# Kernel tuning notes

Hardware: AMD Instinct MI355X
Metric: run time of the kernel (lower is better)

Reference implementation:

```python
import jax, jax.numpy as jnp
import numpy as np

N, E = 50000, 800000
NODE_IN, EDGE_IN = 32, 16
EMB, GEMB = 128, 128
H, C, L, B = 4, 32, 2, 8   # heads, per-head dim, layers, graphs
GAT_IN = NODE_IN + EMB      # skip_conn=True
NEG_SLOPE = 0.2
EPS = 1e-5


def layernorm(x, g, b):
    m = jnp.mean(x, -1, keepdims=True)
    v = jnp.mean((x - m) ** 2, -1, keepdims=True)
    return (x - m) / jnp.sqrt(v + EPS) * g + b


def setup_inputs() -> dict:
    key = jax.random.key(0)
    ks = jax.random.split(key, 24)
    s = 0.05
    return {
        "x": jax.random.normal(ks[0], (N, NODE_IN), jnp.float32),
        "edge_attr": jax.random.normal(ks[1], (E, EDGE_IN), jnp.float32),
        "W_in": jax.random.normal(ks[2], (NODE_IN, EMB), jnp.float32) * s,
        "b_in": jnp.zeros((EMB,), jnp.float32),
        "W_src": jax.random.normal(ks[3], (L, GAT_IN, H * C), jnp.float32) * s,
        "W_edge": jax.random.normal(ks[4], (L, EDGE_IN, H * C), jnp.float32) * s,
        "att_src": jax.random.normal(ks[5], (L, H, C), jnp.float32) * s,
        "att_dst": jax.random.normal(ks[6], (L, H, C), jnp.float32) * s,
        "att_edge": jax.random.normal(ks[7], (L, H, C), jnp.float32) * s,
        "gat_bias": jnp.zeros((L, H * C), jnp.float32),
        "ln_gamma": jnp.ones((L, EMB), jnp.float32),
        "ln_beta": jnp.zeros((L, EMB), jnp.float32),
        "W_out": jax.random.normal(ks[8], (EMB, EMB), jnp.float32) * s,
        "b_out": jnp.zeros((EMB,), jnp.float32),
        "ln_out_gamma": jnp.ones((EMB,), jnp.float32),
        "ln_out_beta": jnp.zeros((EMB,), jnp.float32),
        "W_g": jax.random.normal(ks[9], (EMB, GEMB), jnp.float32) * s,
        "b_g": jnp.zeros((GEMB,), jnp.float32),
        "g_gamma": jnp.ones((GEMB,), jnp.float32),
        "g_beta": jnp.zeros((GEMB,), jnp.float32),
        "edge_index": jax.random.randint(ks[10], (2, E), 0, N, jnp.int32),
        "batch": jnp.sort(jax.random.randint(ks[11], (N,), 0, B, jnp.int32)),
    }


def reference(x, edge_attr, W_in, b_in, W_src, W_edge, att_src, att_dst, att_edge,
              gat_bias, ln_gamma, ln_beta, W_out, b_out, ln_out_gamma, ln_out_beta,
              W_g, b_g, g_gamma, g_beta, edge_index, batch):
    # PyG GATConv adds self-loops with edge_attr fill_value='mean'
    loop = jnp.arange(N, dtype=edge_index.dtype)
    src = jnp.concatenate([edge_index[0], loop])   # [E2]
    dst = jnp.concatenate([edge_index[1], loop])   # [E2]
    ea = jnp.concatenate([edge_attr, jnp.broadcast_to(edge_attr.mean(0), (N, EDGE_IN))], 0)

    h = jax.nn.relu(x @ W_in + b_in)  # [N, EMB]
    for l in range(L):
        inp = jnp.concatenate([x, h], -1)                   # skip connection [N, GAT_IN]
        xs = (inp @ W_src[l]).reshape(N, H, C)              # projected nodes
        a_s = jnp.einsum('nhc,hc->nh', xs, att_src[l])
        a_d = jnp.einsum('nhc,hc->nh', xs, att_dst[l])
        ee = (ea @ W_edge[l]).reshape(-1, H, C)             # [E2, H, C]
        a_e = jnp.einsum('ehc,hc->eh', ee, att_edge[l])
        alpha = jax.nn.leaky_relu(a_s[src] + a_d[dst] + a_e, NEG_SLOPE)  # [E2, H]
        # segment softmax over incoming edges of each destination node
        amax = jax.ops.segment_max(alpha, dst, num_segments=N)
        ex = jnp.exp(alpha - amax[dst])
        denom = jax.ops.segment_sum(ex, dst, num_segments=N)
        w = ex / (denom[dst] + 1e-16)
        msg = xs[src] * w[:, :, None]                        # [E2, H, C]
        out = jax.ops.segment_sum(msg, dst, num_segments=N).reshape(N, H * C) + gat_bias[l]
        h = jax.nn.elu(layernorm(out, ln_gamma[l], ln_beta[l]))

    g = layernorm(jax.nn.relu(h @ W_g + b_g), g_gamma, g_beta)
    gsum = jax.ops.segment_sum(g, batch, num_segments=B)
    cnt = jax.ops.segment_sum(jnp.ones((N, 1), g.dtype), batch, num_segments=B)
    graph_embeddings = gsum / jnp.maximum(cnt, 1.0)

    node_embeddings = layernorm(jax.nn.relu(h @ W_out + b_out), ln_out_gamma, ln_out_beta)
    return node_embeddings, graph_embeddings
```

## Files before the change

### kernel.cpp

```cpp
#include <hip/hip_runtime.h>

#define N_NODES 50000
#define N_EDGES 800000
#define E2      850000
#define NODE_IN 32
#define EDGE_IN 16
#define EMB     128
#define GAT_IN  160
#define NLAYER  2
#define NGRAPH  8
#define NB32    1563
#define NB64    782
#define EB      3321
#define LOG2E   1.44269504088896340736f

#define NBUCK   98
#define CHUNK   4096
#define NCHUNK  208

#define GWT_SRC0 0
#define GWT_SRC1 20480
#define GWT_OUT  40960
#define GWT_G    57344
#define GWT_TOT  73728

typedef short bf16x8 __attribute__((ext_vector_type(8)));
typedef float f32x4 __attribute__((ext_vector_type(4)));

__device__ __forceinline__ unsigned int f2bf(float f) {
    unsigned int u = __float_as_uint(f);
    return (u + 0x7FFFu + ((u >> 16) & 1u)) >> 16;
}
__device__ __forceinline__ float bf2f(unsigned int h) {
    return __uint_as_float(h << 16);
}
__device__ __forceinline__ unsigned int pack2bf(float a, float b) {
    return f2bf(a) | (f2bf(b) << 16);
}

__global__ void zero_kernel(float* __restrict__ p, int n) {
    int i = blockIdx.x * blockDim.x + threadIdx.x;
    int stride = gridDim.x * blockDim.x;
    for (; i < n; i += stride) p[i] = 0.f;
}

__global__ __launch_bounds__(256) void mega_kernel(
    const int* __restrict__ edge_index, const float* __restrict__ edge_attr,
    const float* __restrict__ x, const float* __restrict__ W_in,
    const float* __restrict__ b_in,
    const float* __restrict__ Wsrc, const float* __restrict__ Wout,
    const float* __restrict__ Wg,
    int* __restrict__ hist, float* __restrict__ meta,
    unsigned int* __restrict__ h_bf, unsigned int* __restrict__ x_bf,
    unsigned short* __restrict__ gwt) {
    __shared__ float smem[32 * NODE_IN];
    int b = blockIdx.x, t = threadIdx.x;

    if (b < NCHUNK) {
        int* lh = (int*)smem;
        if (t < NBUCK) lh[t] = 0;
        __syncthreads();
        int c0 = b * CHUNK;
#pragma unroll
        for (int i = 0; i < CHUNK / 256; i++) {
            int e = c0 + i * 256 + t;
            if (e < E2) {
                int dst = (e < N_EDGES) ? edge_index[N_EDGES + e] : (e - N_EDGES);
                atomicAdd(&lh[dst >> 9], 1);
            }
        }
        __syncthreads();
        if (t < NBUCK) hist[t * NCHUNK + b] = lh[t];
    } else if (b < NCHUNK + 512) {
        if (t < 16) smem[t] = 0.f;
        __syncthreads();
        int gid = (b - NCHUNK) * 256 + t;
        int q = gid & 3;
        const float4* ea4 = (const float4*)edge_attr;
        float4 s = make_float4(0.f, 0.f, 0.f, 0.f);
        for (int j = gid; j < N_EDGES * 4; j += 512 * 256) {
            float4 v = ea4[j];
            s.x += v.x; s.y += v.y; s.z += v.z; s.w += v.w;
        }
        atomicAdd(&smem[q * 4 + 0], s.x);
        atomicAdd(&smem[q * 4 + 1], s.y);
        atomicAdd(&smem[q * 4 + 2], s.z);
        atomicAdd(&smem[q * 4 + 3], s.w);
        __syncthreads();
        if (t < 16) atomicAdd(&meta[t], smem[t]);
    } else if (b < NCHUNK + 512 + NB32) {
        float (*inp)[NODE_IN] = (float (*)[NODE_IN])smem;
        int n0 = (b - NCHUNK - 512) * 32;
        for (int i = t; i < 32 * NODE_IN; i += 256) {
            int r = i >> 5, c = i & 31;
            int n = min(n0 + r, N_NODES - 1);
            inp[r][c] = x[(size_t)n * NODE_IN + c];
        }
        __syncthreads();
        for (int i = t; i < 32 * 16; i += 256) {
            int r = i >> 4, c = i & 15;
            int n = n0 + r;
            if (n < N_NODES) x_bf[(size_t)n * 16 + c] = pack2bf(inp[r][2 * c], inp[r][2 * c + 1]);
        }
        int wave = t >> 6, lane = t & 63;
        int c0 = lane * 2, c1 = c0 + 1;
        const float2* W2 = (const float2*)W_in;
        float acc[8][2];
#pragma unroll
        for (int j = 0; j < 8; j++) { acc[j][0] = b_in[c0]; acc[j][1] = b_in[c1]; }
#pragma unroll 2
        for (int k4 = 0; k4 < NODE_IN / 4; k4++) {
            float4 v[8];
#pragma unroll
            for (int j = 0; j < 8; j++) v[j] = *(const float4*)&inp[wave * 8 + j][k4 * 4];
#pragma unroll
            for (int kk = 0; kk < 4; kk++) {
                float2 w = W2[(k4 * 4 + kk) * 64 + lane];
#pragma unroll
                for (int j = 0; j < 8; j++) {
                    float vv = (&v[j].x)[kk];
                    acc[j][0] += vv * w.x;
                    acc[j][1] += vv * w.y;
                }
            }
        }
#pragma unroll
        for (int j = 0; j < 8; j++) {
            int n = n0 + wave * 8 + j;
            if (n < N_NODES)
                h_bf[(size_t)n * 64 + lane] = pack2bf(fmaxf(acc[j][0], 0.f), fmaxf(acc[j][1], 0.f));
        }
    } else {
        int g = (b - NCHUNK - 512 - NB32) * 256 + t;
        const float* Wm;
        int base, gg;
        if (g < 5120) {
            int l = g / 2560;
            gg = g - l * 2560;
            Wm = Wsrc + (size_t)l * GAT_IN * EMB;
            base = l * 20480;
        } else if (g < 7168) {
            gg = g - 5120;
            Wm = Wout;
            base = GWT_OUT;
        } else {
            gg = g - 7168;
            Wm = Wg;
            base = GWT_G;
        }
        int lane = gg & 63, tmp = gg >> 6;
        int nt = tmp & 7, kc = tmp >> 3;
        int quad = lane >> 4, l16 = lane & 15;
        int col = nt * 16 + l16, k0 = kc * 32 + quad * 8;
        unsigned int u[4];
#pragma unroll
        for (int j = 0; j < 4; j++)
            u[j] = pack2bf(Wm[(size_t)(k0 + 2 * j) * EMB + col],
                           Wm[(size_t)(k0 + 2 * j + 1) * EMB + col]);
        *(uint4*)(gwt + base + (size_t)gg * 8) = make_uint4(u[0], u[1], u[2], u[3]);
    }
}

__global__ __launch_bounds__(256) void bucket_scan_kernel(int* __restrict__ hist,
                                                          int* __restrict__ btot) {
    __shared__ int sm[256];
    int k = blockIdx.x, t = threadIdx.x;
    int v = (t < NCHUNK) ? hist[k * NCHUNK + t] : 0;
    sm[t] = v;
    __syncthreads();
#pragma unroll
    for (int d = 1; d < 256; d <<= 1) {
        int u = (t >= d) ? sm[t - d] : 0;
        __syncthreads();
        sm[t] += u;
        __syncthreads();
    }
    if (t < NCHUNK) hist[k * NCHUNK + t] = sm[t] - v;
    if (t == 255) btot[k] = sm[255];
}

__global__ __launch_bounds__(256) void base_prep_kernel(const int* __restrict__ btot,
                                                        int* __restrict__ bucket_base,
                                                        const float* __restrict__ W_edge,
                                                        const float* __restrict__ att_edge,
                                                        float* __restrict__ meta) {
    __shared__ int sm[256];
    int t = threadIdx.x;
    int v = (t < NBUCK) ? btot[t] : 0;
    sm[t] = v;
    __syncthreads();
#pragma unroll
    for (int d = 1; d < 256; d <<= 1) {
        int u = (t >= d) ? sm[t - d] : 0;
        __syncthreads();
        sm[t] += u;
        __syncthreads();
    }
    if (t < NBUCK) bucket_base[t] = sm[t] - v;
    if (t == NBUCK - 1) bucket_base[NBUCK] = sm[t];

    if (t < EDGE_IN) meta[t] = meta[t] * (1.0f / (float)N_EDGES);
    __syncthreads();
    if (t < 128) {
        int l = t >> 6, k = (t >> 2) & 15, h = t & 3;
        const float* w = W_edge + ((size_t)l * EDGE_IN + k) * EMB + h * 32;
        const float* a = att_edge + (size_t)l * EMB + h * 32;
        float acc = 0.f;
#pragma unroll
        for (int c = 0; c < 32; c++) acc += w[c] * a[c];
        meta[16 + (l * 16 + k) * 4 + h] = acc * LOG2E;
    }
    __syncthreads();
    if (t < 8) {
        int l = t >> 2, h = t & 3;
        float acc = 0.f;
#pragma unroll
        for (int k = 0; k < EDGE_IN; k++) acc += meta[k] * meta[16 + (l * 16 + k) * 4 + h];
        meta[144 + t] = acc;
    }
}

__global__ __launch_bounds__(256) void scatter_bucket_kernel(const int* __restrict__ edge_index,
                                                             const int* __restrict__ hist,
                                                             const int* __restrict__ bucket_base,
                                                             int2* __restrict__ brec) {
    __shared__ int cur[NBUCK];
    int b = blockIdx.x, t = threadIdx.x;
    if (t < NBUCK) cur[t] = bucket_base[t] + hist[t * NCHUNK + b];
    __syncthreads();
    int c0 = b * CHUNK;
#pragma unroll
    for (int i = 0; i < CHUNK / 256; i++) {
        int e = c0 + i * 256 + t;
        if (e < E2) {
            int src, dst;
            if (e < N_EDGES) {
                src = edge_index[e];
                dst = edge_index[N_EDGES + e];
            } else {
                src = dst = e - N_EDGES;
            }
            int pos = atomicAdd(&cur[dst >> 9], 1);
            brec[pos] = make_int2(src | ((dst & 511) << 16), e);
        }
    }
}

__global__ __launch_bounds__(512) void local_sort_kernel(const int* __restrict__ bucket_base,
                                                         const int2* __restrict__ brec,
                                                         int* __restrict__ off,
                                                         int2* __restrict__ perm) {
    __shared__ int lh[512];
    __shared__ int sm[512];
    int k = blockIdx.x, t = threadIdx.x;
    int base = bucket_base[k], end = bucket_base[k + 1], cnt = end - base;
    lh[t] = 0;
    __syncthreads();
    for (int i = t; i < cnt; i += 512) {
        int2 r = brec[base + i];
        atomicAdd(&lh[(r.x >> 16) & 511], 1);
    }
    __syncthreads();
    int v = lh[t];
    sm[t] = v;
    __syncthreads();
#pragma unroll
    for (int d = 1; d < 512; d <<= 1) {
        int u = (t >= d) ? sm[t - d] : 0;
        __syncthreads();
        sm[t] += u;
        __syncthreads();
    }
    int excl = sm[t] - v;
    int dst = (k << 9) + t;
    if (dst < N_NODES) off[dst] = base + excl;
    if (k == NBUCK - 1 && t == 0) off[N_NODES] = E2;
    lh[t] = excl;
    __syncthreads();
    for (int i = t; i < cnt; i += 512) {
        int2 r = brec[base + i];
        int dl = (r.x >> 16) & 511;
        int p = atomicAdd(&lh[dl], 1);
        perm[base + p] = make_int2(r.x & 0xFFFF, r.y);
    }
}

__global__ __launch_bounds__(256) void compute_ae_kernel(const int2* __restrict__ perm,
                                                         const float* __restrict__ edge_attr,
                                                         const float* __restrict__ meta,
                                                         int* __restrict__ csr_src,
                                                         float* __restrict__ csr_ae0,
                                                         float* __restrict__ csr_ae1) {
    __shared__ float Ml[128];
    __shared__ float loop_ae[8];
    int t = threadIdx.x;
    if (t < 128) Ml[t] = meta[16 + t];
    if (t < 8) loop_ae[t] = meta[144 + t];
    __syncthreads();
    int p = blockIdx.x * 256 + t;
    if (p >= E2) return;
    int2 pe = perm[p];
    int src = pe.x, e = pe.y;
    csr_src[p] = src;
    float ae[2][4];
    if (e < N_EDGES) {
        const float4* r4 = (const float4*)(edge_attr + (size_t)e * EDGE_IN);
#pragma unroll
        for (int l = 0; l < 2; l++)
#pragma unroll
            for (int hh = 0; hh < 4; hh++) ae[l][hh] = 0.f;
#pragma unroll
        for (int q = 0; q < 4; q++) {
            float4 v = r4[q];
#pragma unroll
            for (int l = 0; l < 2; l++) {
                const float* M = Ml + l * 64;
#pragma unroll
                for (int hh = 0; hh < 4; hh++) {
                    ae[l][hh] += v.x * M[(4 * q + 0) * 4 + hh] + v.y * M[(4 * q + 1) * 4 + hh] +
                                 v.z * M[(4 * q + 2) * 4 + hh] + v.w * M[(4 * q + 3) * 4 + hh];
                }
            }
        }
    } else {
#pragma unroll
        for (int l = 0; l < 2; l++)
#pragma unroll
            for (int hh = 0; hh < 4; hh++) ae[l][hh] = loop_ae[l * 4 + hh];
    }
    *(float4*)(csr_ae0 + (size_t)p * 4) = make_float4(ae[0][0], ae[0][1], ae[0][2], ae[0][3]);
    *(float4*)(csr_ae1 + (size_t)p * 4) = make_float4(ae[1][0], ae[1][1], ae[1][2], ae[1][3]);
}

template <int K, int MODE>
__global__ __launch_bounds__(256) void dense_mfma_kernel(
    const unsigned int* __restrict__ xbf, const unsigned int* __restrict__ hbf,
    const unsigned short* __restrict__ gwt, const float* __restrict__ bias,
    const float* __restrict__ v1, const float* __restrict__ v2,
    const int* __restrict__ batch,
    unsigned int* __restrict__ xs_out, float* __restrict__ a_s, float* __restrict__ a_d,
    float* __restrict__ out_nodes, float* __restrict__ gsum, float* __restrict__ gcnt) {
    constexpr int CLS = 132;
    __shared__ __align__(16) float cl[64 * CLS];
    __shared__ float red[(MODE != 0) ? 64 : 1][8];
    __shared__ float locw[(MODE == 2) ? 4 : 1][2][EMB];
    __shared__ int bids[(MODE == 2) ? 64 : 1];

    int t = threadIdx.x;
    int n0 = blockIdx.x * 64;
    if (MODE == 2 && t < 64) bids[t] = batch[min(n0 + t, N_NODES - 1)];

    int wave = t >> 6, lane = t & 63;
    int quad = lane >> 4, l16 = lane & 15;
    int arow = min(n0 + wave * 16 + l16, N_NODES - 1);
    const bf16x8* B = (const bf16x8*)gwt;
    f32x4 acc[8];
#pragma unroll
    for (int i = 0; i < 8; i++) acc[i] = (f32x4){0.f, 0.f, 0.f, 0.f};
#pragma unroll
    for (int kc = 0; kc < K / 32; kc++) {
        bf16x8 af;
        if (MODE == 0 && kc == 0) {
            af = *(const bf16x8*)(xbf + (size_t)arow * 16 + quad * 4);
        } else {
            int hk = ((MODE == 0) ? (kc - 1) : kc) * 16;
            af = *(const bf16x8*)(hbf + (size_t)arow * 64 + hk + quad * 4);
        }
#pragma unroll
        for (int nt = 0; nt < 8; nt++) {
            bf16x8 bfv = B[(kc * 8 + nt) * 64 + lane];
            acc[nt] = __builtin_amdgcn_mfma_f32_16x16x32_bf16(af, bfv, acc[nt], 0, 0, 0);
        }
    }
#pragma unroll
    for (int nt = 0; nt < 8; nt++) {
#pragma unroll
        for (int i = 0; i < 4; i++) {
            int r = wave * 16 + quad * 4 + i;
            cl[r * CLS + nt * 16 + l16] = acc[nt][i];
        }
    }
    __syncthreads();

    int p = t & 3, r = t >> 2;
    int n = n0 + r;
    const float4* c4 = (const float4*)(cl + r * CLS + p * 32);

    if (MODE == 0) {
        const float4* s4 = (const float4*)(v1 + p * 32);
        const float4* d4 = (const float4*)(v2 + p * 32);
        if (n < N_NODES) {
            float s_ = 0.f, d_ = 0.f;
#pragma unroll
            for (int i = 0; i < 8; i++) {
                float4 cv = c4[i], sv = s4[i], dv = d4[i];
                s_ += cv.x * sv.x + cv.y * sv.y + cv.z * sv.z + cv.w * sv.w;
                d_ += cv.x * dv.x + cv.y * dv.y + cv.z * dv.z + cv.w * dv.w;
                uint2 pk = make_uint2(pack2bf(cv.x, cv.y), pack2bf(cv.z, cv.w));
                *(uint2*)(xs_out + (size_t)n * 64 + p * 16 + 2 * i) = pk;
            }
            a_s[(size_t)n * 4 + p] = s_ * LOG2E;
            a_d[(size_t)n * 4 + p] = d_ * LOG2E;
        }
    } else {
        const float4* b4 = (const float4*)(bias + p * 32);
        float vals[32];
        float s_ = 0.f, q_ = 0.f;
#pragma unroll
        for (int i = 0; i < 8; i++) {
            float4 cv = c4[i], bv = b4[i];
            float w0 = fmaxf(cv.x + bv.x, 0.f), w1 = fmaxf(cv.y + bv.y, 0.f);
            float w2 = fmaxf(cv.z + bv.z, 0.f), w3 = fmaxf(cv.w + bv.w, 0.f);
            vals[4 * i] = w0; vals[4 * i + 1] = w1; vals[4 * i + 2] = w2; vals[4 * i + 3] = w3;
            s_ += w0 + w1 + w2 + w3;
            q_ += w0 * w0 + w1 * w1 + w2 * w2 + w3 * w3;
        }
        red[r][p] = s_;
        red[r][4 + p] = q_;
        __syncthreads();
        float sm = red[r][0] + red[r][1] + red[r][2] + red[r][3];
        float sq = red[r][4] + red[r][5] + red[r][6] + red[r][7];
        float mean = sm * (1.f / EMB);
        float var = sq * (1.f / EMB) - mean * mean;
        float rstd = rsqrtf(var + 1e-5f);
        const float4* g4 = (const float4*)(v1 + p * 32);
        const float4* be4 = (const float4*)(v2 + p * 32);
#pragma unroll
        for (int i = 0; i < 8; i++) {
            float4 gv = g4[i], bv = be4[i];
            vals[4 * i]     = (vals[4 * i]     - mean) * rstd * gv.x + bv.x;
            vals[4 * i + 1] = (vals[4 * i + 1] - mean) * rstd * gv.y + bv.y;
            vals[4 * i + 2] = (vals[4 * i + 2] - mean) * rstd * gv.z + bv.z;
            vals[4 * i + 3] = (vals[4 * i + 3] - mean) * rstd * gv.w + bv.w;
        }
        if (MODE == 1) {
            if (n < N_NODES) {
                float* op = out_nodes + (size_t)n * EMB + p * 32;
#pragma unroll
                for (int i = 0; i < 8; i++)
                    *(float4*)(op + 4 * i) = make_float4(vals[4 * i], vals[4 * i + 1],
                                                         vals[4 * i + 2], vals[4 * i + 3]);
            }
        } else {
            int nvalid = min(64, N_NODES - n0);
            int bmin = bids[0], bmax = bids[nvalid - 1];
            int bid = bids[r];
            bool inA = (bid == bmin) && (n < N_NODES);
            bool inB = (bid == bmax) && (bmax != bmin) && (n < N_NODES);
            if (n < N_NODES && bid != bmin && bid != bmax) {
#pragma unroll
                for (int i = 0; i < 32; i++)
                    atomicAdd(&gsum[(size_t)bid * EMB + p * 32 + i], vals[i]);
            }
#pragma unroll
            for (int g = 0; g < 2; g++) {
                bool m = g ? inB : inA;
#pragma unroll
                for (int i = 0; i < 32; i++) {
                    float v = m ? vals[i] : 0.f;
                    v += __shfl_xor(v, 4, 64);
                    v += __shfl_xor(v, 8, 64);
                    v += __shfl_xor(v, 16, 64);
                    v += __shfl_xor(v, 32, 64);
                    if ((lane >> 2) == 0) locw[wave][g][(lane & 3) * 32 + i] = v;
                }
            }
            __syncthreads();
            if (t < 128) {
                float sA = locw[0][0][t] + locw[1][0][t] + locw[2][0][t] + locw[3][0][t];
                atomicAdd(&gsum[(size_t)bmin * EMB + t], sA);
                if (bmax != bmin) {
                    float sB = locw[0][1][t] + locw[1][1][t] + locw[2][1][t] + locw[3][1][t];
                    atomicAdd(&gsum[(size_t)bmax * EMB + t], sB);
                }
            } else if (t == 255) {
                int cA = 0, cB = 0;
                for (int rr = 0; rr < nvalid; rr++) {
                    int bb = bids[rr];
                    if (bb == bmin) cA++;
                    else if (bb == bmax) cB++;
                    else atomicAdd(&gcnt[bb], 1.f);
                }
                atomicAdd(&gcnt[bmin], (float)cA);
                if (bmax != bmin && cB > 0) atomicAdd(&gcnt[bmax], (float)cB);
            }
        }
    }
}

__global__ __launch_bounds__(256) void gat_gather_kernel(const int* __restrict__ off,
                                                         const int* __restrict__ csr_src,
                                                         const float* __restrict__ csr_ae,
                                                         const unsigned int* __restrict__ xs,
                                                         const float* __restrict__ a_s,
                                                         const float* __restrict__ a_d,
                                                         const float* __restrict__ bias_l,
                                                         const float* __restrict__ gamma_l,
                                                         const float* __restrict__ beta_l,
                                                         unsigned int* __restrict__ h_bf) {
    int t = threadIdx.x, wave = t >> 6, lane = t & 63;
    int n = blockIdx.x * 4 + wave;
    int g = lane >> 4, l16 = lane & 15;
    int h = l16 >> 2;
    float ad = a_d[n * 4 + h];
    int p0 = __builtin_amdgcn_readfirstlane(off[n]);
    int p1 = __builtin_amdgcn_readfirstlane(off[n + 1]);
    float den = 0.f;
    float acc[8];
#pragma unroll
    for (int j = 0; j < 8; j++) acc[j] = 0.f;

#define ACCUM8(X, EX)                                          \
    acc[0] += EX * __uint_as_float(X.x << 16);                 \
    acc[1] += EX * __uint_as_float(X.x & 0xFFFF0000u);         \
    acc[2] += EX * __uint_as_float(X.y << 16);                 \
    acc[3] += EX * __uint_as_float(X.y & 0xFFFF0000u);         \
    acc[4] += EX * __uint_as_float(X.z << 16);                 \
    acc[5] += EX * __uint_as_float(X.z & 0xFFFF0000u);         \
    acc[6] += EX * __uint_as_float(X.w << 16);                 \
    acc[7] += EX * __uint_as_float(X.w & 0xFFFF0000u);

    int pb = p0;
    for (; pb + 8 <= p1; pb += 8) {
        int pA = pb + g, pB = pA + 4;
        int sA = csr_src[pA], sB = csr_src[pB];
        float aeA = csr_ae[pA * 4 + h];
        float aeB = csr_ae[pB * 4 + h];
        float asA = a_s[sA * 4 + h];
        float asB = a_s[sB * 4 + h];
        uint4 xA = *(const uint4*)(xs + (sA * 64 + l16 * 4));
        uint4 xB = *(const uint4*)(xs + (sB * 64 + l16 * 4));
        float alA = asA + ad + aeA;
        alA = fmaxf(alA, 0.2f * alA);
        float exA = exp2f(alA);
        float alB = asB + ad + aeB;
        alB = fmaxf(alB, 0.2f * alB);
        float exB = exp2f(alB);
        den += exA + exB;
        ACCUM8(xA, exA)
        ACCUM8(xB, exB)
    }
    if (pb < p1) {
        int plast = p1 - 1;
        int qA = pb + g, qB = pb + 4 + g;
        int pA = min(qA, plast), pB = min(qB, plast);
        int sA = csr_src[pA], sB = csr_src[pB];
        float aeA = csr_ae[pA * 4 + h];
        float aeB = csr_ae[pB * 4 + h];
        float asA = a_s[sA * 4 + h];
        float asB = a_s[sB * 4 + h];
        uint4 xA = *(const uint4*)(xs + (sA * 64 + l16 * 4));
        uint4 xB = *(const uint4*)(xs + (sB * 64 + l16 * 4));
        float alA = asA + ad + aeA;
        alA = fmaxf(alA, 0.2f * alA);
        float exA = (qA <= plast) ? exp2f(alA) : 0.f;
        float alB = asB + ad + aeB;
        alB = fmaxf(alB, 0.2f * alB);
        float exB = (qB <= plast) ? exp2f(alB) : 0.f;
        den += exA + exB;
        ACCUM8(xA, exA)
        ACCUM8(xB, exB)
    }
#undef ACCUM8

#pragma unroll
    for (int j = 0; j < 8; j++) {
        acc[j] += __shfl_xor(acc[j], 16, 64);
        acc[j] += __shfl_xor(acc[j], 32, 64);
    }
    den += __shfl_xor(den, 16, 64);
    den += __shfl_xor(den, 32, 64);

    float dinv = 1.0f / (den + 1e-16f);
    int c0 = l16 * 8;
    const float4* b4 = (const float4*)(bias_l + c0);
    float4 bv0 = b4[0], bv1 = b4[1];
    float v[8];
    v[0] = acc[0] * dinv + bv0.x; v[1] = acc[1] * dinv + bv0.y;
    v[2] = acc[2] * dinv + bv0.z; v[3] = acc[3] * dinv + bv0.w;
    v[4] = acc[4] * dinv + bv1.x; v[5] = acc[5] * dinv + bv1.y;
    v[6] = acc[6] * dinv + bv1.z; v[7] = acc[7] * dinv + bv1.w;
    float sm = 0.f, sq = 0.f;
#pragma unroll
    for (int j = 0; j < 8; j++) { sm += v[j]; sq += v[j] * v[j]; }
#pragma unroll
    for (int o = 1; o <= 8; o <<= 1) {
        sm += __shfl_xor(sm, o, 64);
        sq += __shfl_xor(sq, o, 64);
    }
    float mean = sm * (1.f / EMB);
    float var = sq * (1.f / EMB) - mean * mean;
    float rstd = rsqrtf(var + 1e-5f);
    const float4* g4 = (const float4*)(gamma_l + c0);
    const float4* be4 = (const float4*)(beta_l + c0);
    float4 gv0 = g4[0], gv1 = g4[1], bev0 = be4[0], bev1 = be4[1];
    float y[8];
    y[0] = (v[0] - mean) * rstd * gv0.x + bev0.x;
    y[1] = (v[1] - mean) * rstd * gv0.y + bev0.y;
    y[2] = (v[2] - mean) * rstd * gv0.z + bev0.z;
    y[3] = (v[3] - mean) * rstd * gv0.w + bev0.w;
    y[4] = (v[4] - mean) * rstd * gv1.x + bev1.x;
    y[5] = (v[5] - mean) * rstd * gv1.y + bev1.y;
    y[6] = (v[6] - mean) * rstd * gv1.z + bev1.z;
    y[7] = (v[7] - mean) * rstd * gv1.w + bev1.w;
#pragma unroll
    for (int j = 0; j < 8; j++) y[j] = y[j] > 0.f ? y[j] : __expf(y[j]) - 1.f;
    if (g == 0) {
        uint4 o4;
        o4.x = pack2bf(y[0], y[1]);
        o4.y = pack2bf(y[2], y[3]);
        o4.z = pack2bf(y[4], y[5]);
        o4.w = pack2bf(y[6], y[7]);
        *(uint4*)(h_bf + (size_t)n * 64 + l16 * 4) = o4;
    }
}

__global__ void graph_out_kernel(const float* __restrict__ gsum, const float* __restrict__ gcnt,
                                 float* __restrict__ out) {
    int i = blockIdx.x * blockDim.x + threadIdx.x;
    if (i >= NGRAPH * EMB) return;
    int b = i >> 7;
    float c = fmaxf(gcnt[b], 1.f);
    out[(size_t)N_NODES * EMB + i] = gsum[i] / c;
}

extern "C" void kernel_launch(void* const* d_in, const int* in_sizes, int n_in,
                              void* d_out, int out_size, void* d_ws, size_t ws_size,
                              hipStream_t stream) {
    (void)in_sizes; (void)n_in; (void)out_size; (void)ws_size;
    const float* x         = (const float*)d_in[0];
    const float* edge_attr = (const float*)d_in[1];
    const float* W_in      = (const float*)d_in[2];
    const float* b_in      = (const float*)d_in[3];
    const float* W_src     = (const float*)d_in[4];
    const float* W_edge    = (const float*)d_in[5];
    const float* att_src   = (const float*)d_in[6];
    const float* att_dst   = (const float*)d_in[7];
    const float* att_edge  = (const float*)d_in[8];
    const float* gat_bias  = (const float*)d_in[9];
    const float* ln_gamma  = (const float*)d_in[10];
    const float* ln_beta   = (const float*)d_in[11];
    const float* W_out     = (const float*)d_in[12];
    const float* b_out     = (const float*)d_in[13];
    const float* ln_og     = (const float*)d_in[14];
    const float* ln_ob     = (const float*)d_in[15];
    const float* W_g       = (const float*)d_in[16];
    const float* b_g       = (const float*)d_in[17];
    const float* g_gamma   = (const float*)d_in[18];
    const float* g_beta    = (const float*)d_in[19];
    const int* edge_index  = (const int*)d_in[20];
    const int* batch       = (const int*)d_in[21];
    float* out = (float*)d_out;

    float* ws              = (float*)d_ws;
    unsigned int* h_bf     = (unsigned int*)ws;
    unsigned int* xs       = h_bf + (size_t)N_NODES * 64;
    unsigned int* x_bf     = xs + (size_t)N_NODES * 64;
    float* a_s             = (float*)(x_bf + (size_t)N_NODES * 16);
    float* a_d             = a_s + (size_t)N_NODES * 4;
    float* csr_ae          = a_d + (size_t)N_NODES * 4;
    unsigned short* gwt    = (unsigned short*)(csr_ae + (size_t)2 * E2 * 4);
    float* meta            = (float*)(gwt + GWT_TOT);
    float* gsum            = meta + 152;
    float* gcnt            = gsum + NGRAPH * EMB;
    int*   off             = (int*)(gcnt + NGRAPH);
    int*   csr_src         = off + N_NODES + 2;
    int2*  brec            = (int2*)(csr_src + E2);
    int*   hist            = (int*)(brec + E2);
    int*   btot            = hist + NBUCK * NCHUNK;
    int*   bucket_base     = btot + NBUCK;
    int2*  perm            = (int2*)xs;

    zero_kernel<<<8, 256, 0, stream>>>(meta, 152 + NGRAPH * EMB + NGRAPH);
    mega_kernel<<<NCHUNK + 512 + NB32 + 36, 256, 0, stream>>>(
        edge_index, edge_attr, x, W_in, b_in, W_src, W_out, W_g,
        hist, meta, h_bf, x_bf, gwt);

    bucket_scan_kernel<<<NBUCK, 256, 0, stream>>>(hist, btot);
    base_prep_kernel<<<1, 256, 0, stream>>>(btot, bucket_base, W_edge, att_edge, meta);
    scatter_bucket_kernel<<<NCHUNK, 256, 0, stream>>>(edge_index, hist, bucket_base, brec);
    local_sort_kernel<<<NBUCK, 512, 0, stream>>>(bucket_base, brec, off, perm);
    compute_ae_kernel<<<EB, 256, 0, stream>>>(perm, edge_attr, meta,
                                              csr_src, csr_ae, csr_ae + (size_t)E2 * 4);

    for (int l = 0; l < NLAYER; l++) {
        dense_mfma_kernel<GAT_IN, 0><<<NB64, 256, 0, stream>>>(
            x_bf, h_bf, gwt + (l ? GWT_SRC1 : GWT_SRC0), nullptr,
            att_src + (size_t)l * EMB, att_dst + (size_t)l * EMB, nullptr,
            xs, a_s, a_d, nullptr, nullptr, nullptr);
        gat_gather_kernel<<<N_NODES / 4, 256, 0, stream>>>(
            off, csr_src, csr_ae + (size_t)l * E2 * 4, xs, a_s, a_d,
            gat_bias + (size_t)l * EMB, ln_gamma + (size_t)l * EMB,
            ln_beta + (size_t)l * EMB, h_bf);
    }

    dense_mfma_kernel<EMB, 1><<<NB64, 256, 0, stream>>>(
        nullptr, h_bf, gwt + GWT_OUT, b_out, ln_og, ln_ob, nullptr,
        nullptr, nullptr, nullptr, out, nullptr, nullptr);
    dense_mfma_kernel<EMB, 2><<<NB64, 256, 0, stream>>>(
        nullptr, h_bf, gwt + GWT_G, b_g, g_gamma, g_beta, batch,
        nullptr, nullptr, nullptr, nullptr, gsum, gcnt);
    graph_out_kernel<<<4, 256, 0, stream>>>(gsum, gcnt, out);
}
```

Before: 403.7 us.

## Fuse edge-attr projection into local sort, merge output dense kernels, prefetch gather indices

Folds the per-edge attention-term computation into the local sort kernel so the intermediate perm array is never written or reread, removing one launch. The two final dense MFMA kernels (node output and graph pooling) are combined into one launch that picks its mode per block. The gather loop now software-prefetches the next iteration's source indices and edge terms to hide latency. The fused sort kernel runs with only 98 blocks, so the edge-attr work gets much less parallelism than the old 3321-block kernel did.

```diff
diff --git a/kernel.cpp b/kernel.cpp
--- a/kernel.cpp
+++ b/kernel.cpp
@@ -11,7 +11,6 @@
 #define NGRAPH  8
 #define NB32    1563
 #define NB64    782
-#define EB      3321
 #define LOG2E   1.44269504088896340736f
 
 #define NBUCK   98
@@ -248,11 +247,19 @@
 
 __global__ __launch_bounds__(512) void local_sort_kernel(const int* __restrict__ bucket_base,
                                                          const int2* __restrict__ brec,
+                                                         const float* __restrict__ edge_attr,
+                                                         const float* __restrict__ meta,
                                                          int* __restrict__ off,
-                                                         int2* __restrict__ perm) {
+                                                         int* __restrict__ csr_src,
+                                                         float* __restrict__ csr_ae0,
+                                                         float* __restrict__ csr_ae1) {
     __shared__ int lh[512];
     __shared__ int sm[512];
+    __shared__ float Ml[128];
+    __shared__ float loop_ae[8];
     int k = blockIdx.x, t = threadIdx.x;
+    if (t < 128) Ml[t] = meta[16 + t];
+    if (t < 8) loop_ae[t] = meta[144 + t];
     int base = bucket_base[k], end = bucket_base[k + 1], cnt = end - base;
     lh[t] = 0;
     __syncthreads();
@@ -281,55 +288,39 @@
         int2 r = brec[base + i];
         int dl = (r.x >> 16) & 511;
         int p = atomicAdd(&lh[dl], 1);
-        perm[base + p] = make_int2(r.x & 0xFFFF, r.y);
-    }
-}
-
-__global__ __launch_bounds__(256) void compute_ae_kernel(const int2* __restrict__ perm,
-                                                         const float* __restrict__ edge_attr,
-                                                         const float* __restrict__ meta,
-                                                         int* __restrict__ csr_src,
-                                                         float* __restrict__ csr_ae0,
-                                                         float* __restrict__ csr_ae1) {
-    __shared__ float Ml[128];
-    __shared__ float loop_ae[8];
-    int t = threadIdx.x;
-    if (t < 128) Ml[t] = meta[16 + t];
-    if (t < 8) loop_ae[t] = meta[144 + t];
-    __syncthreads();
-    int p = blockIdx.x * 256 + t;
-    if (p >= E2) return;
-    int2 pe = perm[p];
-    int src = pe.x, e = pe.y;
-    csr_src[p] = src;
-    float ae[2][4];
-    if (e < N_EDGES) {
-        const float4* r4 = (const float4*)(edge_attr + (size_t)e * EDGE_IN);
-#pragma unroll
-        for (int l = 0; l < 2; l++)
-#pragma unroll
-            for (int hh = 0; hh < 4; hh++) ae[l][hh] = 0.f;
-#pragma unroll
-        for (int q = 0; q < 4; q++) {
-            float4 v = r4[q];
-#pragma unroll
-            for (int l = 0; l < 2; l++) {
-                const float* M = Ml + l * 64;
-#pragma unroll
-                for (int hh = 0; hh < 4; hh++) {
-                    ae[l][hh] += v.x * M[(4 * q + 0) * 4 + hh] + v.y * M[(4 * q + 1) * 4 + hh] +
-                                 v.z * M[(4 * q + 2) * 4 + hh] + v.w * M[(4 * q + 3) * 4 + hh];
+        int pos = base + p;
+        int src = r.x & 0xFFFF;
+        int e = r.y;
+        csr_src[pos] = src;
+        float ae[2][4];
+        if (e < N_EDGES) {
+            const float4* r4 = (const float4*)(edge_attr + (size_t)e * EDGE_IN);
+#pragma unroll
+            for (int l = 0; l < 2; l++)
+#pragma unroll
+                for (int hh = 0; hh < 4; hh++) ae[l][hh] = 0.f;
+#pragma unroll
+            for (int q = 0; q < 4; q++) {
+                float4 vv = r4[q];
+#pragma unroll
+                for (int l = 0; l < 2; l++) {
+                    const float* M = Ml + l * 64;
+#pragma unroll
+                    for (int hh = 0; hh < 4; hh++) {
+                        ae[l][hh] += vv.x * M[(4 * q + 0) * 4 + hh] + vv.y * M[(4 * q + 1) * 4 + hh] +
+                                     vv.z * M[(4 * q + 2) * 4 + hh] + vv.w * M[(4 * q + 3) * 4 + hh];
+                    }
                 }
             }
-        }
-    } else {
-#pragma unroll
-        for (int l = 0; l < 2; l++)
-#pragma unroll
-            for (int hh = 0; hh < 4; hh++) ae[l][hh] = loop_ae[l * 4 + hh];
-    }
-    *(float4*)(csr_ae0 + (size_t)p * 4) = make_float4(ae[0][0], ae[0][1], ae[0][2], ae[0][3]);
-    *(float4*)(csr_ae1 + (size_t)p * 4) = make_float4(ae[1][0], ae[1][1], ae[1][2], ae[1][3]);
+        } else {
+#pragma unroll
+            for (int l = 0; l < 2; l++)
+#pragma unroll
+                for (int hh = 0; hh < 4; hh++) ae[l][hh] = loop_ae[l * 4 + hh];
+        }
+        *(float4*)(csr_ae0 + (size_t)pos * 4) = make_float4(ae[0][0], ae[0][1], ae[0][2], ae[0][3]);
+        *(float4*)(csr_ae1 + (size_t)pos * 4) = make_float4(ae[1][0], ae[1][1], ae[1][2], ae[1][3]);
+    }
 }
 
 template <int K, int MODE>
@@ -339,21 +330,37 @@
     const float* __restrict__ v1, const float* __restrict__ v2,
     const int* __restrict__ batch,
     unsigned int* __restrict__ xs_out, float* __restrict__ a_s, float* __restrict__ a_d,
-    float* __restrict__ out_nodes, float* __restrict__ gsum, float* __restrict__ gcnt) {
+    float* __restrict__ out_nodes, float* __restrict__ gsum, float* __restrict__ gcnt,
+    const float* __restrict__ bias2, const float* __restrict__ v1b,
+    const float* __restrict__ v2b) {
     constexpr int CLS = 132;
     __shared__ __align__(16) float cl[64 * CLS];
     __shared__ float red[(MODE != 0) ? 64 : 1][8];
-    __shared__ float locw[(MODE == 2) ? 4 : 1][2][EMB];
-    __shared__ int bids[(MODE == 2) ? 64 : 1];
+    __shared__ float locw[(MODE == 3) ? 4 : 1][2][EMB];
+    __shared__ int bids[(MODE == 3) ? 64 : 1];
 
     int t = threadIdx.x;
-    int n0 = blockIdx.x * 64;
-    if (MODE == 2 && t < 64) bids[t] = batch[min(n0 + t, N_NODES - 1)];
+    int mode = MODE;
+    int blk = blockIdx.x;
+    if (MODE == 3) {
+        mode = (blockIdx.x < NB64) ? 1 : 2;
+        blk = (mode == 1) ? blockIdx.x : blockIdx.x - NB64;
+    }
+    int n0 = blk * 64;
+    const unsigned short* gw = gwt;
+    const float* bias_ = bias;
+    const float* v1_ = v1;
+    const float* v2_ = v2;
+    if (MODE == 3 && mode == 2) {
+        gw = gwt + (GWT_G - GWT_OUT);
+        bias_ = bias2; v1_ = v1b; v2_ = v2b;
+    }
+    if (MODE == 3 && mode == 2 && t < 64) bids[t] = batch[min(n0 + t, N_NODES - 1)];
 
     int wave = t >> 6, lane = t & 63;
     int quad = lane >> 4, l16 = lane & 15;
     int arow = min(n0 + wave * 16 + l16, N_NODES - 1);
-    const bf16x8* B = (const bf16x8*)gwt;
+    const bf16x8* B = (const bf16x8*)gw;
     f32x4 acc[8];
 #pragma unroll
     for (int i = 0; i < 8; i++) acc[i] = (f32x4){0.f, 0.f, 0.f, 0.f};
@@ -387,8 +394,8 @@
     const float4* c4 = (const float4*)(cl + r * CLS + p * 32);
 
     if (MODE == 0) {
-        const float4* s4 = (const float4*)(v1 + p * 32);
-        const float4* d4 = (const float4*)(v2 + p * 32);
+        const float4* s4 = (const float4*)(v1_ + p * 32);
+        const float4* d4 = (const float4*)(v2_ + p * 32);
         if (n < N_NODES) {
             float s_ = 0.f, d_ = 0.f;
 #pragma unroll
@@ -403,7 +410,7 @@
             a_d[(size_t)n * 4 + p] = d_ * LOG2E;
         }
     } else {
-        const float4* b4 = (const float4*)(bias + p * 32);
+        const float4* b4 = (const float4*)(bias_ + p * 32);
         float vals[32];
         float s_ = 0.f, q_ = 0.f;
 #pragma unroll
@@ -423,8 +430,8 @@
         float mean = sm * (1.f / EMB);
         float var = sq * (1.f / EMB) - mean * mean;
         float rstd = rsqrtf(var + 1e-5f);
-        const float4* g4 = (const float4*)(v1 + p * 32);
-        const float4* be4 = (const float4*)(v2 + p * 32);
+        const float4* g4 = (const float4*)(v1_ + p * 32);
+        const float4* be4 = (const float4*)(v2_ + p * 32);
 #pragma unroll
         for (int i = 0; i < 8; i++) {
             float4 gv = g4[i], bv = be4[i];
@@ -433,7 +440,7 @@
             vals[4 * i + 2] = (vals[4 * i + 2] - mean) * rstd * gv.z + bv.z;
             vals[4 * i + 3] = (vals[4 * i + 3] - mean) * rstd * gv.w + bv.w;
         }
-        if (MODE == 1) {
+        if (mode == 1) {
             if (n < N_NODES) {
                 float* op = out_nodes + (size_t)n * EMB + p * 32;
 #pragma unroll
@@ -520,20 +527,36 @@
     acc[6] += EX * __uint_as_float(X.w << 16);                 \
     acc[7] += EX * __uint_as_float(X.w & 0xFFFF0000u);
 
+    int niter = (p1 - p0) >> 3;
     int pb = p0;
-    for (; pb + 8 <= p1; pb += 8) {
+    int sA = 0, sB = 0;
+    float aeA = 0.f, aeB = 0.f;
+    if (niter > 0) {
         int pA = pb + g, pB = pA + 4;
-        int sA = csr_src[pA], sB = csr_src[pB];
-        float aeA = csr_ae[pA * 4 + h];
-        float aeB = csr_ae[pB * 4 + h];
-        float asA = a_s[sA * 4 + h];
-        float asB = a_s[sB * 4 + h];
-        uint4 xA = *(const uint4*)(xs + (sA * 64 + l16 * 4));
-        uint4 xB = *(const uint4*)(xs + (sB * 64 + l16 * 4));
-        float alA = asA + ad + aeA;
+        sA = csr_src[pA];
+        sB = csr_src[pB];
+        aeA = csr_ae[pA * 4 + h];
+        aeB = csr_ae[pB * 4 + h];
+    }
+    for (int it = 0; it < niter; it++) {
+        int sA0 = sA, sB0 = sB;
+        float aeA0 = aeA, aeB0 = aeB;
+        pb += 8;
+        if (it + 1 < niter) {
+            int pA = pb + g, pB = pA + 4;
+            sA = csr_src[pA];
+            sB = csr_src[pB];
+            aeA = csr_ae[pA * 4 + h];
+            aeB = csr_ae[pB * 4 + h];
+        }
+        float asA = a_s[sA0 * 4 + h];
+        float asB = a_s[sB0 * 4 + h];
+        uint4 xA = *(const uint4*)(xs + (sA0 * 64 + l16 * 4));
+        uint4 xB = *(const uint4*)(xs + (sB0 * 64 + l16 * 4));
+        float alA = asA + ad + aeA0;
         alA = fmaxf(alA, 0.2f * alA);
         float exA = exp2f(alA);
-        float alB = asB + ad + aeB;
+        float alB = asB + ad + aeB0;
         alB = fmaxf(alB, 0.2f * alB);
         float exB = exp2f(alB);
         den += exA + exB;
@@ -544,17 +567,17 @@
         int plast = p1 - 1;
         int qA = pb + g, qB = pb + 4 + g;
         int pA = min(qA, plast), pB = min(qB, plast);
-        int sA = csr_src[pA], sB = csr_src[pB];
-        float aeA = csr_ae[pA * 4 + h];
-        float aeB = csr_ae[pB * 4 + h];
-        float asA = a_s[sA * 4 + h];
-        float asB = a_s[sB * 4 + h];
-        uint4 xA = *(const uint4*)(xs + (sA * 64 + l16 * 4));
-        uint4 xB = *(const uint4*)(xs + (sB * 64 + l16 * 4));
-        float alA = asA + ad + aeA;
+        int tsA = csr_src[pA], tsB = csr_src[pB];
+        float aeA1 = csr_ae[pA * 4 + h];
+        float aeB1 = csr_ae[pB * 4 + h];
+        float asA = a_s[tsA * 4 + h];
+        float asB = a_s[tsB * 4 + h];
+        uint4 xA = *(const uint4*)(xs + (tsA * 64 + l16 * 4));
+        uint4 xB = *(const uint4*)(xs + (tsB * 64 + l16 * 4));
+        float alA = asA + ad + aeA1;
         alA = fmaxf(alA, 0.2f * alA);
         float exA = (qA <= plast) ? exp2f(alA) : 0.f;
-        float alB = asB + ad + aeB;
+        float alB = asB + ad + aeB1;
         alB = fmaxf(alB, 0.2f * alB);
         float exB = (qB <= plast) ? exp2f(alB) : 0.f;
         den += exA + exB;
@@ -669,7 +692,6 @@
     int*   hist            = (int*)(brec + E2);
     int*   btot            = hist + NBUCK * NCHUNK;
     int*   bucket_base     = btot + NBUCK;
-    int2*  perm            = (int2*)xs;
 
     zero_kernel<<<8, 256, 0, stream>>>(meta, 152 + NGRAPH * EMB + NGRAPH);
     mega_kernel<<<NCHUNK + 512 + NB32 + 36, 256, 0, stream>>>(
@@ -679,26 +701,23 @@
     bucket_scan_kernel<<<NBUCK, 256, 0, stream>>>(hist, btot);
     base_prep_kernel<<<1, 256, 0, stream>>>(btot, bucket_base, W_edge, att_edge, meta);
     scatter_bucket_kernel<<<NCHUNK, 256, 0, stream>>>(edge_index, hist, bucket_base, brec);
-    local_sort_kernel<<<NBUCK, 512, 0, stream>>>(bucket_base, brec, off, perm);
-    compute_ae_kernel<<<EB, 256, 0, stream>>>(perm, edge_attr, meta,
-                                              csr_src, csr_ae, csr_ae + (size_t)E2 * 4);
+    local_sort_kernel<<<NBUCK, 512, 0, stream>>>(bucket_base, brec, edge_attr, meta,
+                                                 off, csr_src, csr_ae,
+                                                 csr_ae + (size_t)E2 * 4);
 
     for (int l = 0; l < NLAYER; l++) {
         dense_mfma_kernel<GAT_IN, 0><<<NB64, 256, 0, stream>>>(
             x_bf, h_bf, gwt + (l ? GWT_SRC1 : GWT_SRC0), nullptr,
             att_src + (size_t)l * EMB, att_dst + (size_t)l * EMB, nullptr,
-            xs, a_s, a_d, nullptr, nullptr, nullptr);
+            xs, a_s, a_d, nullptr, nullptr, nullptr, nullptr, nullptr, nullptr);
         gat_gather_kernel<<<N_NODES / 4, 256, 0, stream>>>(
             off, csr_src, csr_ae + (size_t)l * E2 * 4, xs, a_s, a_d,
             gat_bias + (size_t)l * EMB, ln_gamma + (size_t)l * EMB,
             ln_beta + (size_t)l * EMB, h_bf);
     }
 
-    dense_mfma_kernel<EMB, 1><<<NB64, 256, 0, stream>>>(
-        nullptr, h_bf, gwt + GWT_OUT, b_out, ln_og, ln_ob, nullptr,
-        nullptr, nullptr, nullptr, out, nullptr, nullptr);
-    dense_mfma_kernel<EMB, 2><<<NB64, 256, 0, stream>>>(
-        nullptr, h_bf, gwt + GWT_G, b_g, g_gamma, g_beta, batch,
-        nullptr, nullptr, nullptr, nullptr, gsum, gcnt);
+    dense_mfma_kernel<EMB, 3><<<2 * NB64, 256, 0, stream>>>(
+        nullptr, h_bf, gwt + GWT_OUT, b_out, ln_og, ln_ob, batch,
+        nullptr, nullptr, nullptr, out, gsum, gcnt, b_g, g_gamma, g_beta);
     graph_out_kernel<<<4, 256, 0, stream>>>(gsum, gcnt, out);
 }
```

Result: slower. 418.1 us (+3.6%).
